# Kernel tuning notes

Hardware: AMD Instinct MI355X
Metric: run time of the kernel (lower is better)

The kernel has to match this reference:

```python
import jax, jax.numpy as jnp
import numpy as np

N_NODES = 50000
N_EDGES = 800000
N_GRAPHS = 512
F_IN = 16
E_DIM = 64
D = 128          # encoder_dim
L_DIM = 64       # latent_dim
MP_STEPS = 3
S2S_STEPS = 3
NEG_SLOPE = 0.01


def _leaky(v):
    return jax.nn.leaky_relu(v, NEG_SLOPE)


def setup_inputs() -> dict:
    key = jax.random.key(0)
    ks = jax.random.split(key, 24)

    def w(k, fan_in, shape):
        return jax.random.normal(k, shape, jnp.float32) / np.sqrt(fan_in)

    inp = {
        "x": jax.random.normal(ks[0], (N_NODES, F_IN), jnp.float32),
        "edge_index": jax.random.randint(ks[1], (2, N_EDGES), 0, N_NODES, jnp.int64),
        "edge_attr": jax.random.normal(ks[2], (N_EDGES, 4), jnp.float32),
        "batch": jnp.sort(jax.random.randint(ks[3], (N_NODES,), 0, N_GRAPHS, jnp.int64)),
        # embedding: Linear(F_IN -> E_DIM); weights stored [in, out]
        "W_emb": w(ks[4], F_IN, (F_IN, E_DIM)),
        "b_emb": jnp.zeros((E_DIM,), jnp.float32),
        # first: Linear(E_DIM -> D)
        "W_first": w(ks[5], E_DIM, (E_DIM, D)),
        "b_first": jnp.zeros((D,), jnp.float32),
        # SAGEConv: lin_l (aggregated neighbors, with bias), lin_r (root, no bias)
        "W_l": w(ks[6], D, (D, D)),
        "b_l": jnp.zeros((D,), jnp.float32),
        "W_r": w(ks[7], D, (D, D)),
        # GRU (1 layer): gates ordered r,z,n as in torch
        "gru_Wih": w(ks[8], D, (D, 3 * D)),
        "gru_Whh": w(ks[9], D, (D, 3 * D)),
        "gru_bih": jnp.zeros((3 * D,), jnp.float32),
        "gru_bhh": jnp.zeros((3 * D,), jnp.float32),
        # Set2Set LSTM: input 2D -> hidden D; gates ordered i,f,g,o as in torch
        "lstm_Wih": w(ks[10], 2 * D, (2 * D, 4 * D)),
        "lstm_Whh": w(ks[11], D, (D, 4 * D)),
        "lstm_bih": jnp.zeros((4 * D,), jnp.float32),
        "lstm_bhh": jnp.zeros((4 * D,), jnp.float32),
        # linear: Linear(2D -> D), final: Linear(D -> L_DIM)
        "W_lin": w(ks[12], 2 * D, (2 * D, D)),
        "b_lin": jnp.zeros((D,), jnp.float32),
        "W_fin": w(ks[13], D, (D, L_DIM)),
        "b_fin": jnp.zeros((L_DIM,), jnp.float32),
    }
    return inp


def _gru_step(x, h, Wih, Whh, bih, bhh):
    gi = x @ Wih + bih
    gh = h @ Whh + bhh
    ir, iz, inn = jnp.split(gi, 3, axis=-1)
    hr, hz, hn = jnp.split(gh, 3, axis=-1)
    r = jax.nn.sigmoid(ir + hr)
    z = jax.nn.sigmoid(iz + hz)
    n = jnp.tanh(inn + r * hn)
    return (1.0 - z) * n + z * h


def _lstm_step(x, h, c, Wih, Whh, bih, bhh):
    g = x @ Wih + bih + h @ Whh + bhh
    i, f, gg, o = jnp.split(g, 4, axis=-1)
    c_new = jax.nn.sigmoid(f) * c + jax.nn.sigmoid(i) * jnp.tanh(gg)
    h_new = jax.nn.sigmoid(o) * jnp.tanh(c_new)
    return h_new, c_new


def reference(x, edge_index, edge_attr, batch,
              W_emb, b_emb, W_first, b_first,
              W_l, b_l, W_r,
              gru_Wih, gru_Whh, gru_bih, gru_bhh,
              lstm_Wih, lstm_Whh, lstm_bih, lstm_bhh,
              W_lin, b_lin, W_fin, b_fin):
    # edge_attr is ignored (PyG SAGEConv does not use it).
    out = _leaky(x @ W_emb + b_emb)        # [N, E_DIM]
    out = _leaky(out @ W_first + b_first)  # [N, D]
    h = out                                # GRU hidden state [N, D]
    src, dst = edge_index[0], edge_index[1]
    for _ in range(MP_STEPS):
        agg = jax.ops.segment_sum(out[src], dst, num_segments=N_NODES)  # [N, D]
        m = jax.nn.relu(agg @ W_l + b_l + out @ W_r)  # SAGEConv(aggr='add') + root
        out = _gru_step(m, h, gru_Wih, gru_Whh, gru_bih, gru_bhh)
        h = out
    # Set2Set pooling over graphs
    q_star = jnp.zeros((N_GRAPHS, 2 * D), out.dtype)
    hh = jnp.zeros((N_GRAPHS, D), out.dtype)
    cc = jnp.zeros((N_GRAPHS, D), out.dtype)
    for _ in range(S2S_STEPS):
        hh, cc = _lstm_step(q_star, hh, cc, lstm_Wih, lstm_Whh, lstm_bih, lstm_bhh)
        e = jnp.sum(out * hh[batch], axis=-1)                             # [N]
        e_max = jax.ops.segment_max(e, batch, num_segments=N_GRAPHS)      # [B]
        a = jnp.exp(e - e_max[batch])
        s = jax.ops.segment_sum(a, batch, num_segments=N_GRAPHS)
        a = a / (s[batch] + 1e-16)                                        # segment softmax
        r = jax.ops.segment_sum(a[:, None] * out, batch, num_segments=N_GRAPHS)  # [B, D]
        q_star = jnp.concatenate([hh, r], axis=-1)                        # [B, 2D]
    out = _leaky(q_star @ W_lin + b_lin)
    return out @ W_fin + b_fin  # [B, L_DIM]
```

## Files before the change

### kernel.cpp

```cpp
#include <hip/hip_runtime.h>
#include <hip/hip_bf16.h>
#include <math.h>

#define N_NODES 50000
#define N_EDGES 800000
#define N_GRAPHS 512
#define F_IN 16
#define E_DIM 64
#define D 128
#define L_DIM 64
#define NEG_SLOPE 0.01f

#define SCAN_N (N_NODES + 1)
#define NBUCK ((N_NODES + 127) >> 7)
#define EPT 4
#define BFT 1024
#define EPB (BFT * EPT)

typedef __hip_bfloat16 bf16;
typedef unsigned int uint;
typedef unsigned short ushort;
typedef __attribute__((ext_vector_type(8))) short short8;
typedef __attribute__((ext_vector_type(4))) float float4v;

__device__ __forceinline__ float b2f(bf16 v) { return __bfloat162float(v); }
__device__ __forceinline__ bf16  f2b(float v) { return __float2bfloat16(v); }
__device__ __forceinline__ short f2bs(float f) { bf16 b = __float2bfloat16(f); return *reinterpret_cast<short*>(&b); }
__device__ __forceinline__ float bs2f(short s) { return __uint_as_float(((uint)(ushort)s) << 16); }
__device__ __forceinline__ float leaky(float v) { return v > 0.f ? v : NEG_SLOPE * v; }
__device__ __forceinline__ float sigm(float v) { return 1.f / (1.f + expf(-v)); }

__global__ __launch_bounds__(256) void k_signal(float* outp, int n)
{
    int i = blockIdx.x * 256 + threadIdx.x;
    if (i < n) outp[i] = 1.0f;
}

#define NPE 16
__global__ __launch_bounds__(128) void k_embed(
    const float* __restrict__ x, const float* __restrict__ Wemb, const float* __restrict__ bemb,
    const float* __restrict__ Wfirst, const float* __restrict__ bfirst, bf16* __restrict__ out)
{
    __shared__ float xs[NPE][F_IN];
    __shared__ float ys[NPE][E_DIM];
    int t = threadIdx.x;
    int base = blockIdx.x * NPE;

    for (int i = t; i < NPE * F_IN; i += 128)
        xs[i / F_IN][i % F_IN] = x[(size_t)base * F_IN + i];
    __syncthreads();

    if (t < E_DIM) {
        float acc[NPE];
#pragma unroll
        for (int nn = 0; nn < NPE; nn++) acc[nn] = 0.f;
        for (int k = 0; k < F_IN; k++) {
            float w = Wemb[k * E_DIM + t];
#pragma unroll
            for (int nn = 0; nn < NPE; nn++) acc[nn] += xs[nn][k] * w;
        }
        float bb = bemb[t];
#pragma unroll
        for (int nn = 0; nn < NPE; nn++) ys[nn][t] = leaky(acc[nn] + bb);
    }
    __syncthreads();

    {
        float acc[NPE];
#pragma unroll
        for (int nn = 0; nn < NPE; nn++) acc[nn] = 0.f;
        for (int k = 0; k < E_DIM; k++) {
            float w = Wfirst[k * D + t];
#pragma unroll
            for (int nn = 0; nn < NPE; nn++) acc[nn] += ys[nn][k] * w;
        }
        float bb = bfirst[t];
#pragma unroll
        for (int nn = 0; nn < NPE; nn++)
            out[(size_t)(base + nn) * D + t] = f2b(leaky(acc[nn] + bb));
    }
}

__global__ __launch_bounds__(256) void k_bcount(const int* __restrict__ ei, int* __restrict__ bcnt)
{
    __shared__ int lc[NBUCK];
    for (int i = threadIdx.x; i < NBUCK; i += 256) lc[i] = 0;
    __syncthreads();
    int stride = gridDim.x * 256;
    for (int e = blockIdx.x * 256 + threadIdx.x; e < N_EDGES; e += stride) {
        int d = ei[N_EDGES + e];
        d = d < 0 ? 0 : (d >= N_NODES ? N_NODES - 1 : d);
        atomicAdd(&lc[d >> 7], 1);
    }
    __syncthreads();
    for (int i = threadIdx.x; i < NBUCK; i += 256)
        if (lc[i]) atomicAdd(&bcnt[i + 1], lc[i]);
}

__global__ void k_bscan(int* __restrict__ bcnt)
{
    if (threadIdx.x == 0 && blockIdx.x == 0) {
        int run = 0;
        for (int i = 0; i <= NBUCK; i++) { run += bcnt[i]; bcnt[i] = run; }
    }
}

__global__ __launch_bounds__(BFT) void k_bfill2(
    const int* __restrict__ ei, const int* __restrict__ bstart,
    int* __restrict__ bcur, uint* __restrict__ ebuf)
{
    __shared__ int lcnt[NBUCK];
    __shared__ int lbase[NBUCK];
    int t = threadIdx.x;
    int e0 = blockIdx.x * EPB;

    for (int i = t; i < NBUCK; i += BFT) lcnt[i] = 0;
    __syncthreads();

    uint pk[EPT];
    int bb[EPT];
#pragma unroll
    for (int q = 0; q < EPT; q++) {
        int e = e0 + q * BFT + t;
        bb[q] = -1;
        if (e < N_EDGES) {
            int s = ei[e];
            int d = ei[N_EDGES + e];
            s = s < 0 ? 0 : (s >= N_NODES ? N_NODES - 1 : s);
            d = d < 0 ? 0 : (d >= N_NODES ? N_NODES - 1 : d);
            bb[q] = d >> 7;
            pk[q] = ((uint)(d & 127) << 16) | (uint)s;
            atomicAdd(&lcnt[bb[q]], 1);
        }
    }
    __syncthreads();

    for (int i = t; i < NBUCK; i += BFT) {
        int cv = lcnt[i];
        lbase[i] = cv > 0 ? atomicAdd(&bcur[i], cv) : 0;
    }
    __syncthreads();
    for (int i = t; i < NBUCK; i += BFT) lcnt[i] = 0;
    __syncthreads();

#pragma unroll
    for (int q = 0; q < EPT; q++) {
        if (bb[q] >= 0) {
            int pos = lbase[bb[q]] + atomicAdd(&lcnt[bb[q]], 1);
            int slot = bstart[bb[q]] + pos;
            if (slot >= 0 && slot < N_EDGES) ebuf[slot] = pk[q];
        }
    }
}

__global__ __launch_bounds__(256) void k_csr(
    const int* __restrict__ bstart, const uint* __restrict__ ebuf,
    int* __restrict__ offs, int* __restrict__ srcs)
{
    __shared__ int cnt[128];
    __shared__ int loffs[129];
    int b = blockIdx.x, t = threadIdx.x;
    int e0 = bstart[b], e1 = bstart[b + 1];
    if (t < 128) cnt[t] = 0;
    __syncthreads();
    for (int j = e0 + t; j < e1; j += 256)
        atomicAdd(&cnt[(ebuf[j] >> 16) & 127], 1);
    __syncthreads();
    if (t == 0) {
        int run = 0;
        for (int i = 0; i < 128; i++) { loffs[i] = run; run += cnt[i]; }
        loffs[128] = run;
    }
    __syncthreads();
    int n0 = b << 7;
    if (t < 128) {
        int n = n0 + t;
        if (n <= N_NODES) offs[n] = e0 + loffs[t];
        cnt[t] = 0;
    }
    __syncthreads();
    for (int j = e0 + t; j < e1; j += 256) {
        uint pk = ebuf[j];
        int dl = (pk >> 16) & 127;
        int rank = atomicAdd(&cnt[dl], 1);
        int slot = e0 + loffs[dl] + rank;
        if (slot >= 0 && slot < N_EDGES) srcs[slot] = (int)(pk & 0xffffu);
    }
}

__global__ __launch_bounds__(256) void k_gstart(const int* __restrict__ batch, int* __restrict__ gstart)
{
    int g = blockIdx.x * 256 + threadIdx.x;
    if (g > N_GRAPHS) return;
    int lo = 0, hi = N_NODES;
    while (lo < hi) {
        int mid = (lo + hi) >> 1;
        if (batch[mid] < g) lo = mid + 1; else hi = mid;
    }
    gstart[g] = lo;
}

__global__ __launch_bounds__(256) void k_pack_all(
    const float* __restrict__ Wl, const float* __restrict__ Wr,
    const float* __restrict__ gWih, const float* __restrict__ gWhh,
    short* __restrict__ W1p, short* __restrict__ Wihp, short* __restrict__ Whhp)
{
    int tid = blockIdx.x * 256 + threadIdx.x;
    if (tid < 32768) {
        int j = tid & 7, l = (tid >> 3) & 63, frag = tid >> 9;
        int nb = frag & 7, kb = frag >> 3;
        int k = kb * 32 + ((l >> 4) * 8) + j;
        int n = nb * 16 + (l & 15);
        float v = (k < 128) ? Wl[k * D + n] : Wr[(k - 128) * D + n];
        W1p[tid] = f2bs(v);
    } else {
        int id = tid - 32768;
        const float* W = gWih;
        short* Wp = Wihp;
        if (id >= 49152) { id -= 49152; W = gWhh; Wp = Whhp; }
        int j = id & 7, l = (id >> 3) & 63, frag = id >> 9;
        int nb = frag % 24, kb = frag / 24;
        int k = kb * 32 + ((l >> 4) * 8) + j;
        int n = nb * 16 + (l & 15);
        Wp[id] = f2bs(W[k * 384 + n]);
    }
}

__global__ __launch_bounds__(256) void k_gather(
    const bf16* __restrict__ hin, bf16* __restrict__ hagg,
    const int* __restrict__ offs, const int* __restrict__ srcs)
{
    int w = threadIdx.x >> 6, l = threadIdx.x & 63;
    int n = blockIdx.x * 4 + w;
    const ushort* hinu = (const ushort*)hin;
    int j0 = offs[n], j1 = offs[n + 1];
    j0 = j0 < 0 ? 0 : (j0 > N_EDGES ? N_EDGES : j0);
    j1 = j1 < j0 ? j0 : (j1 > N_EDGES ? N_EDGES : j1);

    float lo[8], hi8[8];
#pragma unroll
    for (int i = 0; i < 8; i++) { lo[i] = 0.f; hi8[i] = 0.f; }

    int j = j0;
    for (; j + 7 < j1; j += 8) {
        int ss[8];
        uint vv[8];
#pragma unroll
        for (int i = 0; i < 8; i++) {
            int s = srcs[j + i];
            ss[i] = s < 0 ? 0 : (s >= N_NODES ? N_NODES - 1 : s);
        }
#pragma unroll
        for (int i = 0; i < 8; i++)
            vv[i] = *(const uint*)(hinu + (size_t)ss[i] * D + l * 2);
#pragma unroll
        for (int i = 0; i < 8; i++) {
            lo[i] += __uint_as_float(vv[i] << 16);
            hi8[i] += __uint_as_float(vv[i] & 0xffff0000u);
        }
    }
    for (; j < j1; j++) {
        int s = srcs[j];
        s = s < 0 ? 0 : (s >= N_NODES ? N_NODES - 1 : s);
        uint v = *(const uint*)(hinu + (size_t)s * D + l * 2);
        lo[0] += __uint_as_float(v << 16);
        hi8[0] += __uint_as_float(v & 0xffff0000u);
    }
    float a0 = ((lo[0] + lo[1]) + (lo[2] + lo[3])) + ((lo[4] + lo[5]) + (lo[6] + lo[7]));
    float a1 = ((hi8[0] + hi8[1]) + (hi8[2] + hi8[3])) + ((hi8[4] + hi8[5]) + (hi8[6] + hi8[7]));
    uint ap = ((uint)(ushort)f2bs(a1) << 16) | (ushort)f2bs(a0);
    *(uint*)((ushort*)hagg + (size_t)n * D + l * 2) = ap;
}

#define M_STR 136
__global__ __launch_bounds__(128) void k_sage_gru_mfma(
    const bf16* __restrict__ hin, bf16* __restrict__ hagg_out,
    const short* __restrict__ W1p, const short* __restrict__ Wihp, const short* __restrict__ Whhp,
    const float* __restrict__ bl, const float* __restrict__ bih, const float* __restrict__ bhh)
{
    __shared__ short Msh[64 * M_STR];
    __shared__ short Hsh[64 * M_STR];
    int t = threadIdx.x;
    int w = t >> 6, l = t & 63;
    int base = blockIdx.x * 64;
    const ushort* hinu = (const ushort*)hin;
    const ushort* haggu = (const ushort*)hagg_out;
    ushort* houtu = (ushort*)hagg_out;

    int rA = base + w * 32 + (l & 15);
    int rB = rA + 16;
    int rcA = rA < N_NODES ? rA : N_NODES - 1;
    int rcB = rB < N_NODES ? rB : N_NODES - 1;
    int koff = (l >> 4) * 8;

    short8 afrA[8], afrB[8];
#pragma unroll
    for (int k0 = 0; k0 < 4; k0++) {
        afrA[k0]     = *(const short8*)(haggu + (size_t)rcA * D + k0 * 32 + koff);
        afrB[k0]     = *(const short8*)(haggu + (size_t)rcB * D + k0 * 32 + koff);
        afrA[4 + k0] = *(const short8*)(hinu + (size_t)rcA * D + k0 * 32 + koff);
        afrB[4 + k0] = *(const short8*)(hinu + (size_t)rcB * D + k0 * 32 + koff);
    }

    int mrowA = w * 32 + (l & 15);
    int mrowB = mrowA + 16;
    int crowA = w * 32 + (l >> 4) * 4;
    int crowB = crowA + 16;

#pragma unroll
    for (int k0 = 0; k0 < 4; k0++) {
        *(short8*)&Hsh[mrowA * M_STR + k0 * 32 + koff] = afrA[4 + k0];
        *(short8*)&Hsh[mrowB * M_STR + k0 * 32 + koff] = afrB[4 + k0];
    }

    short8 bA[8], bB[8];
#pragma unroll
    for (int k0 = 0; k0 < 8; k0++)
        bA[k0] = *(const short8*)&W1p[((k0 * 8 + 0) * 64 + l) * 8];
#pragma unroll
    for (int ct = 0; ct < 8; ct++) {
        const short8* bc = (ct & 1) ? bB : bA;
        short8* bn = (ct & 1) ? bA : bB;
        if (ct < 7) {
#pragma unroll
            for (int k0 = 0; k0 < 8; k0++)
                bn[k0] = *(const short8*)&W1p[((k0 * 8 + ct + 1) * 64 + l) * 8];
        }
        float4v accA = {0.f, 0.f, 0.f, 0.f};
        float4v accB = {0.f, 0.f, 0.f, 0.f};
#pragma unroll
        for (int k0 = 0; k0 < 8; k0++) {
            accA = __builtin_amdgcn_mfma_f32_16x16x32_bf16(afrA[k0], bc[k0], accA, 0, 0, 0);
            accB = __builtin_amdgcn_mfma_f32_16x16x32_bf16(afrB[k0], bc[k0], accB, 0, 0, 0);
        }
        float bb = bl[ct * 16 + (l & 15)];
#pragma unroll
        for (int i = 0; i < 4; i++) {
            float vA = accA[i] + bb;
            float vB = accB[i] + bb;
            Msh[(crowA + i) * M_STR + ct * 16 + (l & 15)] = f2bs(vA > 0.f ? vA : 0.f);
            Msh[(crowB + i) * M_STR + ct * 16 + (l & 15)] = f2bs(vB > 0.f ? vB : 0.f);
        }
    }
    __syncthreads();

    short8 amrA[4], amrB[4];
#pragma unroll
    for (int k0 = 0; k0 < 4; k0++) {
        amrA[k0] = *(const short8*)&Msh[mrowA * M_STR + k0 * 32 + koff];
        amrB[k0] = *(const short8*)&Msh[mrowB * M_STR + k0 * 32 + koff];
    }

    short8 iA[4], hA[4], iB[4], hB[4];
#pragma unroll
    for (int k0 = 0; k0 < 4; k0++) {
        iA[k0] = *(const short8*)&Wihp[((k0 * 24 + 0) * 64 + l) * 8];
        hA[k0] = *(const short8*)&Whhp[((k0 * 24 + 0) * 64 + l) * 8];
    }
#pragma unroll
    for (int ct = 0; ct < 8; ct++) {
        int c = ct * 16 + (l & 15);
        float rvA[4], zvA[4], rvB[4], zvB[4];
#pragma unroll
        for (int p = 0; p < 3; p++) {
            int ph = ct * 3 + p;
            const short8* wi = (ph & 1) ? iB : iA;
            const short8* wh = (ph & 1) ? hB : hA;
            short8* win = (ph & 1) ? iA : iB;
            short8* whn = (ph & 1) ? hA : hB;
            if (ph < 23) {
                int pn = ph + 1;
                int ctn = pn / 3, ppn = pn - ctn * 3;
                int nbn = ppn * 8 + ctn;
#pragma unroll
                for (int k0 = 0; k0 < 4; k0++) {
                    win[k0] = *(const short8*)&Wihp[((k0 * 24 + nbn) * 64 + l) * 8];
                    whn[k0] = *(const short8*)&Whhp[((k0 * 24 + nbn) * 64 + l) * 8];
                }
            }
            float4v aiA = {0.f, 0.f, 0.f, 0.f};
            float4v ahA = {0.f, 0.f, 0.f, 0.f};
            float4v aiB = {0.f, 0.f, 0.f, 0.f};
            float4v ahB = {0.f, 0.f, 0.f, 0.f};
#pragma unroll
            for (int k0 = 0; k0 < 4; k0++) {
                aiA = __builtin_amdgcn_mfma_f32_16x16x32_bf16(amrA[k0], wi[k0], aiA, 0, 0, 0);
                ahA = __builtin_amdgcn_mfma_f32_16x16x32_bf16(afrA[4 + k0], wh[k0], ahA, 0, 0, 0);
                aiB = __builtin_amdgcn_mfma_f32_16x16x32_bf16(amrB[k0], wi[k0], aiB, 0, 0, 0);
                ahB = __builtin_amdgcn_mfma_f32_16x16x32_bf16(afrB[4 + k0], wh[k0], ahB, 0, 0, 0);
            }
            float bis = bih[p * 128 + c];
            float bhs = bhh[p * 128 + c];
            if (p == 0) {
#pragma unroll
                for (int i = 0; i < 4; i++) {
                    rvA[i] = sigm(aiA[i] + bis + ahA[i] + bhs);
                    rvB[i] = sigm(aiB[i] + bis + ahB[i] + bhs);
                }
            } else if (p == 1) {
#pragma unroll
                for (int i = 0; i < 4; i++) {
                    zvA[i] = sigm(aiA[i] + bis + ahA[i] + bhs);
                    zvB[i] = sigm(aiB[i] + bis + ahB[i] + bhs);
                }
            } else {
#pragma unroll
                for (int i = 0; i < 4; i++) {
                    int gA = base + crowA + i;
                    float h0A = bs2f(Hsh[(crowA + i) * M_STR + c]);
                    float nA = tanhf(aiA[i] + bis + rvA[i] * (ahA[i] + bhs));
                    if (gA < N_NODES)
                        houtu[(size_t)gA * D + c] = (ushort)f2bs((1.f - zvA[i]) * nA + zvA[i] * h0A);
                    int gB = base + crowB + i;
                    float h0B = bs2f(Hsh[(crowB + i) * M_STR + c]);
                    float nB = tanhf(aiB[i] + bis + rvB[i] * (ahB[i] + bhs));
                    if (gB < N_NODES)
                        houtu[(size_t)gB * D + c] = (ushort)f2bs((1.f - zvB[i]) * nB + zvB[i] * h0B);
                }
            }
        }
    }
}

#define POOL_CAP 1024
#define LG2 2
__global__ __launch_bounds__(1024) void k_s2s(
    const float* __restrict__ Wih, const float* __restrict__ Whh,
    const float* __restrict__ bih, const float* __restrict__ bhh,
    const bf16* __restrict__ h, const int* __restrict__ gstart,
    float* __restrict__ qstar, float* __restrict__ hh, float* __restrict__ cc, int first)
{
    int g0 = blockIdx.x * LG2;
    int t = threadIdx.x;
    __shared__ float qs[LG2][2 * D];
    __shared__ float hs[LG2][D];
    __shared__ float part[2][LG2][512];
    __shared__ float hnew[LG2][D];
    __shared__ float e_lds[POOL_CAP];
    __shared__ float redM[16], redS[16];
    __shared__ float rpart[8][D];

    for (int i = t; i < LG2 * 2 * D; i += 1024) {
        int g = i / (2 * D), c = i % (2 * D);
        qs[g][c] = first ? 0.f : qstar[(size_t)(g0 + g) * 2 * D + c];
    }
    for (int i = t; i < LG2 * D; i += 1024) {
        int g = i / D, c = i % D;
        hs[g][c] = first ? 0.f : hh[(size_t)(g0 + g) * D + c];
    }
    __syncthreads();

    int c = t & 511, half = t >> 9;
    float a0 = half ? 0.f : (bih[c] + bhh[c]);
    float a1 = a0;
    int qb = half * 128;
#pragma unroll 4
    for (int i = 0; i < 128; i++) {
        int k = qb + i;
        float wv = Wih[(size_t)k * 512 + c];
        a0 += qs[0][k] * wv;
        a1 += qs[1][k] * wv;
    }
    int hb = half * 64;
#pragma unroll 4
    for (int i = 0; i < 64; i++) {
        int k = hb + i;
        float wv = Whh[(size_t)k * 512 + c];
        a0 += hs[0][k] * wv;
        a1 += hs[1][k] * wv;
    }
    part[half][0][c] = a0;
    part[half][1][c] = a1;
    __syncthreads();

    if (t < LG2 * D) {
        int g = t >> 7, tt = t & 127;
        float gi = part[0][g][tt] + part[1][g][tt];
        float gf = part[0][g][D + tt] + part[1][g][D + tt];
        float gg2 = part[0][g][2 * D + tt] + part[1][g][2 * D + tt];
        float go = part[0][g][3 * D + tt] + part[1][g][3 * D + tt];
        float c_old = first ? 0.f : cc[(size_t)(g0 + g) * D + tt];
        float cn = sigm(gf) * c_old + sigm(gi) * tanhf(gg2);
        float hn = sigm(go) * tanhf(cn);
        cc[(size_t)(g0 + g) * D + tt] = cn;
        hh[(size_t)(g0 + g) * D + tt] = hn;
        qstar[(size_t)(g0 + g) * 2 * D + tt] = hn;
        hnew[g][tt] = hn;
    }
    __syncthreads();

    int w = t >> 6, l = t & 63;
    int dim = t & 127, h8 = t >> 7;
    const ushort* hu = (const ushort*)h;

    for (int gg = 0; gg < LG2; gg++) {
        int g = g0 + gg;
        int s0 = gstart[g], s1 = gstart[g + 1];
        s0 = s0 < 0 ? 0 : (s0 > N_NODES ? N_NODES : s0);
        s1 = s1 < s0 ? s0 : (s1 > N_NODES ? N_NODES : s1);
        int cnt = s1 - s0;

        float hq0 = hnew[gg][l];
        float hq1 = hnew[gg][64 + l];
        float m_run = -INFINITY, s_run = 0.f, racc = 0.f;

        for (int c0 = 0; c0 < cnt; c0 += POOL_CAP) {
            int clen = cnt - c0; if (clen > POOL_CAP) clen = POOL_CAP;

            for (int i = w; i < clen; i += 16) {
                int n = s0 + c0 + i;
                float v = bs2f((short)hu[(size_t)n * D + l]) * hq0
                        + bs2f((short)hu[(size_t)n * D + 64 + l]) * hq1;
#pragma unroll
                for (int off = 32; off > 0; off >>= 1) v += __shfl_down(v, off);
                if (l == 0) e_lds[i] = v;
            }
            __syncthreads();

            float m = -INFINITY;
            for (int i = t; i < clen; i += 1024) m = fmaxf(m, e_lds[i]);
#pragma unroll
            for (int off = 32; off > 0; off >>= 1) m = fmaxf(m, __shfl_down(m, off));
            if (l == 0) redM[w] = m;
            __syncthreads();
            m = -INFINITY;
#pragma unroll
            for (int i = 0; i < 16; i++) m = fmaxf(m, redM[i]);
            float m_new = fmaxf(m_run, m);
            float scale = (m_run == -INFINITY) ? 0.f : expf(m_run - m_new);
            s_run *= scale;
            racc *= scale;
            __syncthreads();

            float s = 0.f;
            for (int i = t; i < clen; i += 1024) {
                float wv = expf(e_lds[i] - m_new);
                e_lds[i] = wv;
                s += wv;
            }
#pragma unroll
            for (int off = 32; off > 0; off >>= 1) s += __shfl_down(s, off);
            if (l == 0) redS[w] = s;
            __syncthreads();
#pragma unroll
            for (int i = 0; i < 16; i++) s_run += redS[i];

            for (int i = h8; i < clen; i += 8)
                racc += e_lds[i] * bs2f((short)hu[(size_t)(s0 + c0 + i) * D + dim]);
            m_run = m_new;
            __syncthreads();
        }

        rpart[h8][dim] = racc;
        __syncthreads();
        if (t < D) {
            float inv = 1.f / (s_run + 1e-16f);
            float r = 0.f;
#pragma unroll
            for (int i = 0; i < 8; i++) r += rpart[i][t];
            qstar[(size_t)g * 2 * D + D + t] = r * inv;
        }
        __syncthreads();
    }
}

__global__ __launch_bounds__(128) void k_final(
    const float* __restrict__ qstar, const float* __restrict__ Wlin, const float* __restrict__ blin,
    const float* __restrict__ Wfin, const float* __restrict__ bfin, float* __restrict__ outp)
{
    int g = blockIdx.x, t = threadIdx.x;
    __shared__ float qs[2 * D], ts[D];
    qs[t] = qstar[(size_t)g * 2 * D + t];
    qs[D + t] = qstar[(size_t)g * 2 * D + D + t];
    __syncthreads();

    float acc = blin[t];
    for (int k = 0; k < 2 * D; k++) acc += qs[k] * Wlin[(size_t)k * D + t];
    ts[t] = leaky(acc);
    __syncthreads();

    if (t < L_DIM) {
        float a2 = bfin[t];
        for (int k = 0; k < D; k++) a2 += ts[k] * Wfin[(size_t)k * L_DIM + t];
        outp[(size_t)g * L_DIM + t] = a2;
    }
}

extern "C" void kernel_launch(void* const* d_in, const int* in_sizes, int n_in,
                              void* d_out, int out_size, void* d_ws, size_t ws_size,
                              hipStream_t stream)
{
    const float* x      = (const float*)d_in[0];
    const int*   ei     = (const int*)d_in[1];
    const int*   batch  = (const int*)d_in[3];
    const float* Wemb   = (const float*)d_in[4];
    const float* bemb   = (const float*)d_in[5];
    const float* Wfirst = (const float*)d_in[6];
    const float* bfirst = (const float*)d_in[7];
    const float* Wl     = (const float*)d_in[8];
    const float* bl     = (const float*)d_in[9];
    const float* Wr     = (const float*)d_in[10];
    const float* gWih   = (const float*)d_in[11];
    const float* gWhh   = (const float*)d_in[12];
    const float* gbih   = (const float*)d_in[13];
    const float* gbhh   = (const float*)d_in[14];
    const float* lWih   = (const float*)d_in[15];
    const float* lWhh   = (const float*)d_in[16];
    const float* lbih   = (const float*)d_in[17];
    const float* lbhh   = (const float*)d_in[18];
    const float* Wlin   = (const float*)d_in[19];
    const float* blin   = (const float*)d_in[20];
    const float* Wfin   = (const float*)d_in[21];
    const float* bfin   = (const float*)d_in[22];
    float* outp = (float*)d_out;

    size_t o = 0;
    char* base = (char*)d_ws;
    auto carve = [&](size_t bytes) { void* p = base + o; o += (bytes + 255) & ~(size_t)255; return p; };
    bf16*  h0     = (bf16*)carve((size_t)N_NODES * D * sizeof(bf16));
    bf16*  h1     = (bf16*)carve((size_t)N_NODES * D * sizeof(bf16));
    int*   offs   = (int*)carve((size_t)SCAN_N * sizeof(int));
    int*   srcs   = (int*)carve((size_t)N_EDGES * sizeof(int));
    int*   bcnt   = (int*)carve((size_t)(NBUCK + 1) * sizeof(int));
    int*   bcur   = (int*)carve((size_t)NBUCK * sizeof(int));
    uint*  ebuf   = (uint*)carve((size_t)N_EDGES * sizeof(uint));
    float* hh     = (float*)carve((size_t)N_GRAPHS * D * sizeof(float));
    float* cc     = (float*)carve((size_t)N_GRAPHS * D * sizeof(float));
    float* qstar  = (float*)carve((size_t)N_GRAPHS * 2 * D * sizeof(float));
    int*   gstart = (int*)carve((size_t)(N_GRAPHS + 1) * sizeof(int));
    short* W1p    = (short*)carve((size_t)256 * 128 * sizeof(short));
    short* Wihp   = (short*)carve((size_t)128 * 384 * sizeof(short));
    short* Whhp   = (short*)carve((size_t)128 * 384 * sizeof(short));
    size_t need = o;

    if (ws_size < need) {
        k_signal<<<(out_size + 255) / 256, 256, 0, stream>>>(outp, out_size);
        return;
    }

    k_embed<<<N_NODES / NPE, 128, 0, stream>>>(x, Wemb, bemb, Wfirst, bfirst, h0);

    k_pack_all<<<(32768 + 98304) / 256, 256, 0, stream>>>(Wl, Wr, gWih, gWhh, W1p, Wihp, Whhp);

    hipMemsetAsync(bcnt, 0, (size_t)((char*)ebuf - (char*)bcnt), stream);
    k_bcount<<<128, 256, 0, stream>>>(ei, bcnt);
    k_bscan<<<1, 64, 0, stream>>>(bcnt);
    k_bfill2<<<(N_EDGES + EPB - 1) / EPB, BFT, 0, stream>>>(ei, bcnt, bcur, ebuf);
    k_csr<<<NBUCK, 256, 0, stream>>>(bcnt, ebuf, offs, srcs);

    k_gstart<<<(N_GRAPHS + 1 + 255) / 256, 256, 0, stream>>>(batch, gstart);

    bf16* hc = h0; bf16* hn = h1;
    for (int s = 0; s < 3; s++) {
        k_gather<<<N_NODES / 4, 256, 0, stream>>>(hc, hn, offs, srcs);
        k_sage_gru_mfma<<<(N_NODES + 63) / 64, 128, 0, stream>>>(
            hc, hn, W1p, Wihp, Whhp, bl, gbih, gbhh);
        bf16* tmp = hc; hc = hn; hn = tmp;
    }

    for (int s = 0; s < 3; s++) {
        k_s2s<<<N_GRAPHS / LG2, 1024, 0, stream>>>(lWih, lWhh, lbih, lbhh,
                                                   hc, gstart, qstar, hh, cc, s == 0);
    }

    k_final<<<N_GRAPHS, 128, 0, stream>>>(qstar, Wlin, blin, Wfin, bfin, outp);
}
```

Baseline: 505.7 us.

## Split SAGE/GRU MFMA kernel column tiles across two wave groups, use fast math

The fused SAGE+GRU MFMA kernel now runs 256 threads per 64-node tile. Each pair of waves splits the 8 output column tiles in half, so every wave does half the MFMA work and weight streaming. To support this, the weight packing layout is reordered so each half's fragments are contiguous and sequential. Separately, sigmoid, tanh and softmax exponentials switch to fast __expf/rcp approximations, trading slight accuracy for fewer instructions. Each row fragment is still loaded by both column-group waves, so A-operand global reads are duplicated.

```diff
diff --git a/kernel.cpp b/kernel.cpp
--- a/kernel.cpp
+++ b/kernel.cpp
@@ -28,7 +28,15 @@
 __device__ __forceinline__ short f2bs(float f) { bf16 b = __float2bfloat16(f); return *reinterpret_cast<short*>(&b); }
 __device__ __forceinline__ float bs2f(short s) { return __uint_as_float(((uint)(ushort)s) << 16); }
 __device__ __forceinline__ float leaky(float v) { return v > 0.f ? v : NEG_SLOPE * v; }
-__device__ __forceinline__ float sigm(float v) { return 1.f / (1.f + expf(-v)); }
+
+__device__ __forceinline__ float frcp(float x) { return __builtin_amdgcn_rcpf(x); }
+__device__ __forceinline__ float sigm(float v) { return frcp(1.f + __expf(-v)); }
+__device__ __forceinline__ float ftanh(float v)
+{
+    v = fminf(15.f, fmaxf(-15.f, v));
+    float a = __expf(2.f * v);
+    return (a - 1.f) * frcp(a + 1.f);
+}
 
 __global__ __launch_bounds__(256) void k_signal(float* outp, int n)
 {
@@ -208,7 +216,7 @@
     int tid = blockIdx.x * 256 + threadIdx.x;
     if (tid < 32768) {
         int j = tid & 7, l = (tid >> 3) & 63, frag = tid >> 9;
-        int nb = frag & 7, kb = frag >> 3;
+        int nb = frag >> 3, kb = frag & 7;
         int k = kb * 32 + ((l >> 4) * 8) + j;
         int n = nb * 16 + (l & 15);
         float v = (k < 128) ? Wl[k * D + n] : Wr[(k - 128) * D + n];
@@ -218,10 +226,11 @@
         const float* W = gWih;
         short* Wp = Wihp;
         if (id >= 49152) { id -= 49152; W = gWhh; Wp = Whhp; }
-        int j = id & 7, l = (id >> 3) & 63, frag = id >> 9;
-        int nb = frag % 24, kb = frag / 24;
-        int k = kb * 32 + ((l >> 4) * 8) + j;
-        int n = nb * 16 + (l & 15);
+        int j = id & 7, l = (id >> 3) & 63, f = id >> 9;
+        int ph = f >> 2, k0 = f & 3;
+        int ct = ph / 3, p = ph - ct * 3;
+        int k = k0 * 32 + ((l >> 4) * 8) + j;
+        int n = p * 128 + ct * 16 + (l & 15);
         Wp[id] = f2bs(W[k * 384 + n]);
     }
 }
@@ -273,7 +282,7 @@
 }
 
 #define M_STR 136
-__global__ __launch_bounds__(128) void k_sage_gru_mfma(
+__global__ __launch_bounds__(256) void k_sage_gru_mfma(
     const bf16* __restrict__ hin, bf16* __restrict__ hagg_out,
     const short* __restrict__ W1p, const short* __restrict__ Wihp, const short* __restrict__ Whhp,
     const float* __restrict__ bl, const float* __restrict__ bih, const float* __restrict__ bhh)
@@ -282,12 +291,13 @@
     __shared__ short Hsh[64 * M_STR];
     int t = threadIdx.x;
     int w = t >> 6, l = t & 63;
+    int rg = w >> 1, cg = w & 1;
     int base = blockIdx.x * 64;
     const ushort* hinu = (const ushort*)hin;
     const ushort* haggu = (const ushort*)hagg_out;
     ushort* houtu = (ushort*)hagg_out;
 
-    int rA = base + w * 32 + (l & 15);
+    int rA = base + rg * 32 + (l & 15);
     int rB = rA + 16;
     int rcA = rA < N_NODES ? rA : N_NODES - 1;
     int rcB = rB < N_NODES ? rB : N_NODES - 1;
@@ -302,29 +312,33 @@
         afrB[4 + k0] = *(const short8*)(hinu + (size_t)rcB * D + k0 * 32 + koff);
     }
 
-    int mrowA = w * 32 + (l & 15);
+    int mrowA = rg * 32 + (l & 15);
     int mrowB = mrowA + 16;
-    int crowA = w * 32 + (l >> 4) * 4;
+    int crowA = rg * 32 + (l >> 4) * 4;
     int crowB = crowA + 16;
 
-#pragma unroll
-    for (int k0 = 0; k0 < 4; k0++) {
-        *(short8*)&Hsh[mrowA * M_STR + k0 * 32 + koff] = afrA[4 + k0];
-        *(short8*)&Hsh[mrowB * M_STR + k0 * 32 + koff] = afrB[4 + k0];
-    }
-
+    if (cg == 0) {
+#pragma unroll
+        for (int k0 = 0; k0 < 4; k0++) {
+            *(short8*)&Hsh[mrowA * M_STR + k0 * 32 + koff] = afrA[4 + k0];
+            *(short8*)&Hsh[mrowB * M_STR + k0 * 32 + koff] = afrB[4 + k0];
+        }
+    }
+
+    const short* w1 = W1p + cg * 16384;
     short8 bA[8], bB[8];
 #pragma unroll
     for (int k0 = 0; k0 < 8; k0++)
-        bA[k0] = *(const short8*)&W1p[((k0 * 8 + 0) * 64 + l) * 8];
-#pragma unroll
-    for (int ct = 0; ct < 8; ct++) {
-        const short8* bc = (ct & 1) ? bB : bA;
-        short8* bn = (ct & 1) ? bA : bB;
-        if (ct < 7) {
+        bA[k0] = *(const short8*)&w1[k0 * 512 + l * 8];
+#pragma unroll
+    for (int cti = 0; cti < 4; cti++) {
+        int ct = cg * 4 + cti;
+        const short8* bc = (cti & 1) ? bB : bA;
+        short8* bn = (cti & 1) ? bA : bB;
+        if (cti < 3) {
 #pragma unroll
             for (int k0 = 0; k0 < 8; k0++)
-                bn[k0] = *(const short8*)&W1p[((k0 * 8 + ct + 1) * 64 + l) * 8];
+                bn[k0] = *(const short8*)&w1[(cti + 1) * 4096 + k0 * 512 + l * 8];
         }
         float4v accA = {0.f, 0.f, 0.f, 0.f};
         float4v accB = {0.f, 0.f, 0.f, 0.f};
@@ -351,31 +365,31 @@
         amrB[k0] = *(const short8*)&Msh[mrowB * M_STR + k0 * 32 + koff];
     }
 
+    const short* wip = Wihp + cg * 24576;
+    const short* whp = Whhp + cg * 24576;
     short8 iA[4], hA[4], iB[4], hB[4];
 #pragma unroll
     for (int k0 = 0; k0 < 4; k0++) {
-        iA[k0] = *(const short8*)&Wihp[((k0 * 24 + 0) * 64 + l) * 8];
-        hA[k0] = *(const short8*)&Whhp[((k0 * 24 + 0) * 64 + l) * 8];
-    }
-#pragma unroll
-    for (int ct = 0; ct < 8; ct++) {
+        iA[k0] = *(const short8*)&wip[k0 * 512 + l * 8];
+        hA[k0] = *(const short8*)&whp[k0 * 512 + l * 8];
+    }
+#pragma unroll
+    for (int cti = 0; cti < 4; cti++) {
+        int ct = cg * 4 + cti;
         int c = ct * 16 + (l & 15);
         float rvA[4], zvA[4], rvB[4], zvB[4];
 #pragma unroll
         for (int p = 0; p < 3; p++) {
-            int ph = ct * 3 + p;
-            const short8* wi = (ph & 1) ? iB : iA;
-            const short8* wh = (ph & 1) ? hB : hA;
-            short8* win = (ph & 1) ? iA : iB;
-            short8* whn = (ph & 1) ? hA : hB;
-            if (ph < 23) {
-                int pn = ph + 1;
-                int ctn = pn / 3, ppn = pn - ctn * 3;
-                int nbn = ppn * 8 + ctn;
+            int phl = cti * 3 + p;
+            const short8* wi = (phl & 1) ? iB : iA;
+            const short8* wh = (phl & 1) ? hB : hA;
+            short8* win = (phl & 1) ? iA : iB;
+            short8* whn = (phl & 1) ? hA : hB;
+            if (phl < 11) {
 #pragma unroll
                 for (int k0 = 0; k0 < 4; k0++) {
-                    win[k0] = *(const short8*)&Wihp[((k0 * 24 + nbn) * 64 + l) * 8];
-                    whn[k0] = *(const short8*)&Whhp[((k0 * 24 + nbn) * 64 + l) * 8];
+                    win[k0] = *(const short8*)&wip[(phl + 1) * 2048 + k0 * 512 + l * 8];
+                    whn[k0] = *(const short8*)&whp[(phl + 1) * 2048 + k0 * 512 + l * 8];
                 }
             }
             float4v aiA = {0.f, 0.f, 0.f, 0.f};
@@ -408,12 +422,12 @@
                 for (int i = 0; i < 4; i++) {
                     int gA = base + crowA + i;
                     float h0A = bs2f(Hsh[(crowA + i) * M_STR + c]);
-                    float nA = tanhf(aiA[i] + bis + rvA[i] * (ahA[i] + bhs));
+                    float nA = ftanh(aiA[i] + bis + rvA[i] * (ahA[i] + bhs));
                     if (gA < N_NODES)
                         houtu[(size_t)gA * D + c] = (ushort)f2bs((1.f - zvA[i]) * nA + zvA[i] * h0A);
                     int gB = base + crowB + i;
                     float h0B = bs2f(Hsh[(crowB + i) * M_STR + c]);
-                    float nB = tanhf(aiB[i] + bis + rvB[i] * (ahB[i] + bhs));
+                    float nB = ftanh(aiB[i] + bis + rvB[i] * (ahB[i] + bhs));
                     if (gB < N_NODES)
                         houtu[(size_t)gB * D + c] = (ushort)f2bs((1.f - zvB[i]) * nB + zvB[i] * h0B);
                 }
@@ -480,8 +494,8 @@
         float gg2 = part[0][g][2 * D + tt] + part[1][g][2 * D + tt];
         float go = part[0][g][3 * D + tt] + part[1][g][3 * D + tt];
         float c_old = first ? 0.f : cc[(size_t)(g0 + g) * D + tt];
-        float cn = sigm(gf) * c_old + sigm(gi) * tanhf(gg2);
-        float hn = sigm(go) * tanhf(cn);
+        float cn = sigm(gf) * c_old + sigm(gi) * ftanh(gg2);
+        float hn = sigm(go) * ftanh(cn);
         cc[(size_t)(g0 + g) * D + tt] = cn;
         hh[(size_t)(g0 + g) * D + tt] = hn;
         qstar[(size_t)(g0 + g) * 2 * D + tt] = hn;
@@ -527,14 +541,14 @@
 #pragma unroll
             for (int i = 0; i < 16; i++) m = fmaxf(m, redM[i]);
             float m_new = fmaxf(m_run, m);
-            float scale = (m_run == -INFINITY) ? 0.f : expf(m_run - m_new);
+            float scale = (m_run == -INFINITY) ? 0.f : __expf(m_run - m_new);
             s_run *= scale;
             racc *= scale;
             __syncthreads();
 
             float s = 0.f;
             for (int i = t; i < clen; i += 1024) {
-                float wv = expf(e_lds[i] - m_new);
+                float wv = __expf(e_lds[i] - m_new);
                 e_lds[i] = wv;
                 s += wv;
             }
@@ -653,7 +667,7 @@
     bf16* hc = h0; bf16* hn = h1;
     for (int s = 0; s < 3; s++) {
         k_gather<<<N_NODES / 4, 256, 0, stream>>>(hc, hn, offs, srcs);
-        k_sage_gru_mfma<<<(N_NODES + 63) / 64, 128, 0, stream>>>(
+        k_sage_gru_mfma<<<(N_NODES + 63) / 64, 256, 0, stream>>>(
             hc, hn, W1p, Wihp, Whhp, bl, gbih, gbhh);
         bf16* tmp = hc; hc = hn; hn = tmp;
     }
```

Result: no change. 497.8 us (-1.6%).
